# Performance work log

Hardware: AMD Instinct MI355X
Metric: run time of the kernel (lower is better)

The kernel has to match this reference:

```python
import jax, jax.numpy as jnp
import numpy as np

B, S, E = 8, 4096, 512
QKV, H = 512, 8
D = QKV // H  # head_dim = 64
EPS = 1e-6


def setup_inputs() -> dict:
    key = jax.random.key(0)
    ks = jax.random.split(key, 9)
    sc_in = 1.0 / np.sqrt(E)
    sc_qkv = 1.0 / np.sqrt(QKV)
    # Linear weights stored as [in, out] so y = x @ W + b (equivalent to torch x @ W_t.T + b)
    return {
        "x": jax.random.normal(ks[0], (B, S, E), dtype=jnp.float32),
        "Wq": jax.random.uniform(ks[1], (E, QKV), jnp.float32, -sc_in, sc_in),
        "bq": jax.random.uniform(ks[2], (QKV,), jnp.float32, -sc_in, sc_in),
        "Wk": jax.random.uniform(ks[3], (E, QKV), jnp.float32, -sc_in, sc_in),
        "bk": jax.random.uniform(ks[4], (QKV,), jnp.float32, -sc_in, sc_in),
        "Wv": jax.random.uniform(ks[5], (E, QKV), jnp.float32, -sc_in, sc_in),
        "bv": jax.random.uniform(ks[6], (QKV,), jnp.float32, -sc_in, sc_in),
        "Wo": jax.random.uniform(ks[7], (QKV, E), jnp.float32, -sc_qkv, sc_qkv),
        "bo": jax.random.uniform(ks[8], (E,), jnp.float32, -sc_qkv, sc_qkv),
    }


def feature_map(t):
    # elu(x) + 1 (always positive features)
    return jax.nn.elu(t) + 1.0


def reference(x, Wq, bq, Wk, bk, Wv, bv, Wo, bo):
    bs, seqlen, _ = x.shape
    q = (x @ Wq + bq).reshape(bs, seqlen, H, D)
    k = (x @ Wk + bk).reshape(bs, seqlen, H, D)
    v = (x @ Wv + bv).reshape(bs, seqlen, H, D)
    q = feature_map(q)
    k = feature_map(k)
    # kv: [n, h, m, d] -- per-head outer-product accumulation over sequence
    kv = jnp.einsum('nshd,nshm->nhmd', k, v)
    # normalizer z: [n, l, h]
    z = 1.0 / (jnp.einsum('nlhd,nhd->nlh', q, k.sum(axis=1)) + EPS)
    out = jnp.einsum('nlhd,nhmd,nlh->nlhm', q, kv, z)
    out = out.reshape(bs, seqlen, QKV)
    return out @ Wo + bo
```

## Files before the change

### kernel.cpp

```cpp
#include <hip/hip_runtime.h>
#include <hip/hip_bf16.h>


typedef __bf16 bf16x8 __attribute__((ext_vector_type(8)));
typedef float  f32x4  __attribute__((ext_vector_type(4)));

__device__ __forceinline__ float b2f(unsigned short u) {
    unsigned int x = ((unsigned int)u) << 16;
    return __builtin_bit_cast(float, x);
}
__device__ __forceinline__ unsigned short f2b(float f) {
    unsigned int u = __builtin_bit_cast(unsigned int, f);
    unsigned int r = (u + 0x7FFFu + ((u >> 16) & 1u)) >> 16;
    return (unsigned short)r;
}
__device__ __forceinline__ void load_lds16(const unsigned short* g, unsigned short* l) {
    __builtin_amdgcn_global_load_lds(
        (const __attribute__((address_space(1))) void*)g,
        (__attribute__((address_space(3))) void*)l, 16, 0, 0);
}

__global__ void prep_kernel(const float* __restrict__ x,
                            const float* __restrict__ w0, const float* __restrict__ w1,
                            const float* __restrict__ w2, const float* __restrict__ w3,
                            unsigned short* __restrict__ xb, unsigned short* __restrict__ wt) {
    __shared__ float tile[64][65];
    int t = threadIdx.x;
    if (blockIdx.x >= 256) {
        int i = (blockIdx.x - 256) * 256 + t;
        float4 v = ((const float4*)x)[i];
        ushort4 o;
        o.x = f2b(v.x); o.y = f2b(v.y); o.z = f2b(v.z); o.w = f2b(v.w);
        ((ushort4*)xb)[i] = o;
        return;
    }
    int idx = blockIdx.x;
    int bz = idx >> 6, by = (idx >> 3) & 7, bx = idx & 7;
    const float* src = (bz == 0) ? w0 : (bz == 1) ? w1 : (bz == 2) ? w2 : w3;
    unsigned short* dst = wt + (size_t)bz * 512 * 512;
    int rb = by * 64, cb = bx * 64;
    #pragma unroll
    for (int i = 0; i < 16; i++) {
        int c = t + i * 256; int r = c >> 6, cc = c & 63;
        tile[r][cc] = src[(rb + r) * 512 + cb + cc];
    }
    __syncthreads();
    #pragma unroll
    for (int i = 0; i < 16; i++) {
        int c = t + i * 256; int r = c >> 6, cc = c & 63;
        dst[(cb + r) * 512 + rb + cc] = f2b(tile[cc][r]);
    }
}

__device__ __forceinline__ void gemm128(const unsigned short* __restrict__ A,
                                        const unsigned short* __restrict__ Bt,
                                        const float* __restrict__ bias,
                                        unsigned short* __restrict__ Cout,
                                        int mtile, int ntile, bool act) {
    __shared__ __align__(16) unsigned short sA[128 * 64];
    __shared__ __align__(16) unsigned short sB[128 * 64];
    const int tid  = threadIdx.x;
    const int wave = tid >> 6, lane = tid & 63;
    const int wm = wave >> 1, wn = wave & 1;
    const int quad = lane >> 4, l16 = lane & 15;
    const int mbase = mtile * 128, nbase = ntile * 128;
    const int rsub = lane >> 3;
    const int coff = (((lane & 7) ^ rsub) << 3);

    f32x4 acc[4][4];
    #pragma unroll
    for (int i = 0; i < 4; i++)
        #pragma unroll
        for (int j = 0; j < 4; j++) acc[i][j] = (f32x4){0.f, 0.f, 0.f, 0.f};

    for (int kb = 0; kb < 512; kb += 64) {
        #pragma unroll
        for (int t = 0; t < 4; t++) {
            int r0 = t * 32 + wave * 8;
            load_lds16(&A[(size_t)(mbase + r0 + rsub) * 512 + kb + coff], &sA[r0 * 64]);
            load_lds16(&Bt[(size_t)(nbase + r0 + rsub) * 512 + kb + coff], &sB[r0 * 64]);
        }
        __syncthreads();
        #pragma unroll
        for (int ko = 0; ko < 64; ko += 32) {
            bf16x8 af[4], bfr[4];
            int pg = ((quad + (ko >> 3)) ^ (l16 & 7)) << 3;
            #pragma unroll
            for (int f = 0; f < 4; f++)
                af[f] = *(const bf16x8*)&sA[(wm * 64 + f * 16 + l16) * 64 + pg];
            #pragma unroll
            for (int f = 0; f < 4; f++)
                bfr[f] = *(const bf16x8*)&sB[(wn * 64 + f * 16 + l16) * 64 + pg];
            #pragma unroll
            for (int i = 0; i < 4; i++)
                #pragma unroll
                for (int j = 0; j < 4; j++)
                    acc[i][j] = __builtin_amdgcn_mfma_f32_16x16x32_bf16(af[i], bfr[j], acc[i][j], 0, 0, 0);
        }
        __syncthreads();
    }
    #pragma unroll
    for (int i = 0; i < 4; i++) {
        #pragma unroll
        for (int j = 0; j < 4; j++) {
            int gcol = nbase + wn * 64 + j * 16 + l16;
            float bv = bias[gcol];
            #pragma unroll
            for (int r = 0; r < 4; r++) {
                int grow = mbase + wm * 64 + i * 16 + quad * 4 + r;
                float v = acc[i][j][r] + bv;
                if (act) v = v > 0.f ? v + 1.f : __expf(v);
                Cout[(size_t)grow * 512 + gcol] = f2b(v);
            }
        }
    }
}

__global__ __launch_bounds__(256, 4) void gemm_qkv_kernel(
        const unsigned short* __restrict__ xb, const unsigned short* __restrict__ wt,
        const float* __restrict__ bq, const float* __restrict__ bk, const float* __restrict__ bv,
        unsigned short* __restrict__ qb, unsigned short* __restrict__ kb,
        unsigned short* __restrict__ vb) {
    int tensor = blockIdx.x >> 2, ntile = blockIdx.x & 3;
    const unsigned short* Bt = wt + (size_t)tensor * 512 * 512;
    const float* bias = tensor == 0 ? bq : tensor == 1 ? bk : bv;
    unsigned short* out = tensor == 0 ? qb : tensor == 1 ? kb : vb;
    gemm128(xb, Bt, bias, out, blockIdx.y, ntile, tensor < 2);
}

__global__ __launch_bounds__(256) void kv_kernel(
        const unsigned short* __restrict__ kb, const unsigned short* __restrict__ vb,
        float* __restrict__ kvp, float* __restrict__ ksp) {
    int bh = blockIdx.x, sc = blockIdx.y;
    int b = bh >> 3, h = bh & 7;
    const int tid = threadIdx.x;
    int wave = tid >> 6;
    int cell = tid & 63;
    int m0 = (cell >> 3) * 8, d0 = (cell & 7) * 8;
    __shared__ __align__(16) unsigned short sK[32 * 64];
    __shared__ __align__(16) unsigned short sV[32 * 64];
    __shared__ float sAcc[4096];
    __shared__ float sKs[64];
    float acc[8][8];
    #pragma unroll
    for (int i = 0; i < 8; i++)
        #pragma unroll
        for (int j = 0; j < 8; j++) acc[i][j] = 0.f;
    float ks = 0.f;
    size_t gbase = ((size_t)(b * 4096 + sc * 256)) * 512 + h * 64;

    for (int tile = 0; tile < 8; tile++) {
        {
            int r = tid >> 3, cc = (tid & 7) * 8;
            size_t g = gbase + (size_t)(tile * 32 + r) * 512 + cc;
            *(uint4*)&sK[r * 64 + cc] = *(const uint4*)&kb[g];
            *(uint4*)&sV[r * 64 + cc] = *(const uint4*)&vb[g];
        }
        __syncthreads();
        #pragma unroll
        for (int ss = 0; ss < 8; ss++) {
            int s = wave * 8 + ss;
            uint4 kr = *(const uint4*)&sK[s * 64 + d0];
            uint4 vr = *(const uint4*)&sV[s * 64 + m0];
            float kvals[8], vvals[8];
            const unsigned int* kp = (const unsigned int*)&kr;
            const unsigned int* vp = (const unsigned int*)&vr;
            #pragma unroll
            for (int i = 0; i < 4; i++) {
                kvals[2*i]   = __builtin_bit_cast(float, kp[i] << 16);
                kvals[2*i+1] = __builtin_bit_cast(float, kp[i] & 0xFFFF0000u);
                vvals[2*i]   = __builtin_bit_cast(float, vp[i] << 16);
                vvals[2*i+1] = __builtin_bit_cast(float, vp[i] & 0xFFFF0000u);
            }
            #pragma unroll
            for (int i = 0; i < 8; i++)
                #pragma unroll
                for (int j = 0; j < 8; j++)
                    acc[i][j] += vvals[i] * kvals[j];
            ks += b2f(sK[s * 64 + cell]);
        }
        __syncthreads();
    }
    for (int w = 0; w < 4; w++) {
        if (wave == w) {
            #pragma unroll
            for (int i = 0; i < 8; i++)
                #pragma unroll
                for (int j = 0; j < 8; j++) {
                    int idx = (m0 + i) * 64 + d0 + j;
                    if (w == 0) sAcc[idx] = acc[i][j];
                    else        sAcc[idx] += acc[i][j];
                }
            if (w == 0) sKs[cell] = ks;
            else        sKs[cell] += ks;
        }
        __syncthreads();
    }
    float* kvout = kvp + ((size_t)sc * 64 + bh) * 4096;
    #pragma unroll
    for (int i = 0; i < 16; i++) {
        int idx = tid + i * 256;
        kvout[idx] = sAcc[idx];
    }
    if (tid < 64) ksp[((size_t)sc * 64 + bh) * 64 + tid] = sKs[tid];
}

__global__ __launch_bounds__(256) void mid_kernel(
        const float* __restrict__ kvp, const float* __restrict__ ksp,
        const unsigned short* __restrict__ qb,
        unsigned short* __restrict__ kvb, float* __restrict__ zb) {
    int bh = blockIdx.x >> 3, chunk = blockIdx.x & 7;
    int b = bh >> 3, h = bh & 7;
    int tid = threadIdx.x;
    __shared__ float sKsum[64];
    if (tid < 64) {
        float s = 0.f;
        #pragma unroll
        for (int sc = 0; sc < 16; sc++) s += ksp[((size_t)sc * 64 + bh) * 64 + tid];
        sKsum[tid] = s;
    }
    __syncthreads();
    int seg = tid & 7, rsub = tid >> 3;
    float ks8[8];
    #pragma unroll
    for (int j = 0; j < 8; j++) ks8[j] = sKsum[seg * 8 + j];
    #pragma unroll
    for (int p = 0; p < 16; p++) {
        int row = chunk * 512 + p * 32 + rsub;
        uint4 w = *(const uint4*)&qb[((size_t)(b * 4096 + row)) * 512 + h * 64 + seg * 8];
        const unsigned int* qp = (const unsigned int*)&w;
        float d = 0.f;
        #pragma unroll
        for (int i = 0; i < 4; i++) {
            d += __builtin_bit_cast(float, qp[i] << 16)        * ks8[2*i];
            d += __builtin_bit_cast(float, qp[i] & 0xFFFF0000u) * ks8[2*i+1];
        }
        d += __shfl_xor(d, 1, 64);
        d += __shfl_xor(d, 2, 64);
        d += __shfl_xor(d, 4, 64);
        if (seg == 0) zb[h * 32768 + b * 4096 + row] = 1.f / (d + 1e-6f);
    }
    if (chunk == 0) {
        #pragma unroll
        for (int i = 0; i < 4; i++) {
            int idx = (tid + i * 256) * 4;
            float s0 = 0.f, s1 = 0.f, s2 = 0.f, s3 = 0.f;
            #pragma unroll
            for (int sc = 0; sc < 16; sc++) {
                float4 v = *(const float4*)&kvp[((size_t)sc * 64 + bh) * 4096 + idx];
                s0 += v.x; s1 += v.y; s2 += v.z; s3 += v.w;
            }
            ushort4 o; o.x = f2b(s0); o.y = f2b(s1); o.z = f2b(s2); o.w = f2b(s3);
            *(ushort4*)&kvb[(size_t)bh * 4096 + idx] = o;
        }
    }
}

__global__ __launch_bounds__(256, 2) void fused_out_kernel(
        const unsigned short* __restrict__ qb,
        const unsigned short* __restrict__ kvb, const float* __restrict__ zb,
        const unsigned short* __restrict__ wto, const float* __restrict__ bo,
        float* __restrict__ out) {
    __shared__ __align__(16) unsigned short sQ[128 * 64];
    __shared__ __align__(16) unsigned short sWo[128 * 64];
    __shared__ __align__(16) unsigned short sKV[64 * 64];
    __shared__ __align__(16) unsigned short sO1[128 * 64];
    __shared__ float sZ[128];
    const int tid  = threadIdx.x;
    const int wave = tid >> 6, lane = tid & 63;
    const int wm = wave >> 1, wn = wave & 1;
    const int quad = lane >> 4, l16 = lane & 15;
    const int mbase = blockIdx.y * 128, nbase = blockIdx.x * 128;
    const int b = blockIdx.y >> 5;
    const int rsub = lane >> 3;
    const int coff = (((lane & 7) ^ rsub) << 3);

    f32x4 accm[4][4];
    #pragma unroll
    for (int i = 0; i < 4; i++)
        #pragma unroll
        for (int j = 0; j < 4; j++) accm[i][j] = (f32x4){0.f, 0.f, 0.f, 0.f};

    for (int h = 0; h < 8; h++) {
        #pragma unroll
        for (int t = 0; t < 4; t++) {
            int r0 = t * 32 + wave * 8;
            load_lds16(&qb[(size_t)(mbase + r0 + rsub) * 512 + h * 64 + coff], &sQ[r0 * 64]);
            load_lds16(&wto[(size_t)(nbase + r0 + rsub) * 512 + h * 64 + coff], &sWo[r0 * 64]);
        }
        #pragma unroll
        for (int t = 0; t < 2; t++) {
            int r0 = t * 32 + wave * 8;
            load_lds16(&kvb[(size_t)(b * 8 + h) * 4096 + (r0 + rsub) * 64 + coff], &sKV[r0 * 64]);
        }
        if (tid < 128) sZ[tid] = zb[h * 32768 + mbase + tid];
        __syncthreads();
        f32x4 acco[4][2];
        #pragma unroll
        for (int f = 0; f < 4; f++)
            #pragma unroll
            for (int j = 0; j < 2; j++) acco[f][j] = (f32x4){0.f, 0.f, 0.f, 0.f};
        #pragma unroll
        for (int ko = 0; ko < 64; ko += 32) {
            bf16x8 af[4], bfr[2];
            int pg = ((quad + (ko >> 3)) ^ (l16 & 7)) << 3;
            #pragma unroll
            for (int f = 0; f < 4; f++)
                af[f] = *(const bf16x8*)&sQ[(wm * 64 + f * 16 + l16) * 64 + pg];
            #pragma unroll
            for (int j = 0; j < 2; j++)
                bfr[j] = *(const bf16x8*)&sKV[(wn * 32 + j * 16 + l16) * 64 + pg];
            #pragma unroll
            for (int f = 0; f < 4; f++)
                #pragma unroll
                for (int j = 0; j < 2; j++)
                    acco[f][j] = __builtin_amdgcn_mfma_f32_16x16x32_bf16(af[f], bfr[j], acco[f][j], 0, 0, 0);
        }
        #pragma unroll
        for (int f = 0; f < 4; f++)
            #pragma unroll
            for (int j = 0; j < 2; j++)
                #pragma unroll
                for (int r = 0; r < 4; r++) {
                    int row = wm * 64 + f * 16 + quad * 4 + r;
                    int col = wn * 32 + j * 16 + l16;
                    float v = acco[f][j][r] * sZ[row];
                    int g = col >> 3;
                    sO1[row * 64 + ((g ^ (row & 7)) << 3) + (col & 7)] = f2b(v);
                }
        __syncthreads();
        #pragma unroll
        for (int ko = 0; ko < 64; ko += 32) {
            bf16x8 af[4], bfr[4];
            int pg = ((quad + (ko >> 3)) ^ (l16 & 7)) << 3;
            #pragma unroll
            for (int f = 0; f < 4; f++)
                af[f] = *(const bf16x8*)&sO1[(wm * 64 + f * 16 + l16) * 64 + pg];
            #pragma unroll
            for (int f = 0; f < 4; f++)
                bfr[f] = *(const bf16x8*)&sWo[(wn * 64 + f * 16 + l16) * 64 + pg];
            #pragma unroll
            for (int i = 0; i < 4; i++)
                #pragma unroll
                for (int j = 0; j < 4; j++)
                    accm[i][j] = __builtin_amdgcn_mfma_f32_16x16x32_bf16(af[i], bfr[j], accm[i][j], 0, 0, 0);
        }
        __syncthreads();
    }
    #pragma unroll
    for (int i = 0; i < 4; i++)
        #pragma unroll
        for (int j = 0; j < 4; j++) {
            int gcol = nbase + wn * 64 + j * 16 + l16;
            float bv = bo[gcol];
            #pragma unroll
            for (int r = 0; r < 4; r++) {
                int grow = mbase + wm * 64 + i * 16 + quad * 4 + r;
                out[(size_t)grow * 512 + gcol] = accm[i][j][r] + bv;
            }
        }
}

extern "C" void kernel_launch(void* const* d_in, const int* in_sizes, int n_in,
                              void* d_out, int out_size, void* d_ws, size_t ws_size,
                              hipStream_t stream) {
    const float* x  = (const float*)d_in[0];
    const float* Wq = (const float*)d_in[1];
    const float* bq = (const float*)d_in[2];
    const float* Wk = (const float*)d_in[3];
    const float* bk = (const float*)d_in[4];
    const float* Wv = (const float*)d_in[5];
    const float* bv = (const float*)d_in[6];
    const float* Wo = (const float*)d_in[7];
    const float* bo = (const float*)d_in[8];
    float* out = (float*)d_out;

    char* wsb = (char*)d_ws;
    char* ob  = (char*)d_out;
    unsigned short* vb  = (unsigned short*)ob;
    unsigned short* xb  = (unsigned short*)(ob + 33554432ull);
    float*          kvp = (float*)(ob + 33554432ull);
    unsigned short* qb  = (unsigned short*)wsb;
    unsigned short* kb  = (unsigned short*)(wsb + 33554432ull);
    unsigned short* wt  = (unsigned short*)(wsb + 67108864ull);
    float*          ksp = (float*)(wsb + 69206016ull);
    unsigned short* kvb = (unsigned short*)(wsb + 69468160ull);
    float*          zb  = (float*)(wsb + 69992448ull);

    prep_kernel<<<16640, 256, 0, stream>>>(x, Wq, Wk, Wv, Wo, xb, wt);
    gemm_qkv_kernel<<<dim3(12, 256), 256, 0, stream>>>(xb, wt, bq, bk, bv, qb, kb, vb);
    kv_kernel<<<dim3(64, 16), 256, 0, stream>>>(kb, vb, kvp, ksp);
    mid_kernel<<<512, 256, 0, stream>>>(kvp, ksp, qb, kvb, zb);
    fused_out_kernel<<<dim3(4, 256), 256, 0, stream>>>(qb, kvb, zb,
            wt + 3ull * 512 * 512, bo, out);
}
```

Baseline: 288.1 us.

## Store K/V transposed, compute KV outer products with MFMA, remap blocks per XCD

```diff
diff --git a/kernel.cpp b/kernel.cpp
--- a/kernel.cpp
+++ b/kernel.cpp
@@ -52,11 +52,20 @@
     }
 }
 
-__device__ __forceinline__ void gemm128(const unsigned short* __restrict__ A,
-                                        const unsigned short* __restrict__ Bt,
-                                        const float* __restrict__ bias,
-                                        unsigned short* __restrict__ Cout,
-                                        int mtile, int ntile, bool act) {
+__global__ __launch_bounds__(256, 4) void gemm_qkv_kernel(
+        const unsigned short* __restrict__ xb, const unsigned short* __restrict__ wt,
+        const float* __restrict__ bq, const float* __restrict__ bk, const float* __restrict__ bv,
+        unsigned short* __restrict__ qb, unsigned short* __restrict__ kT,
+        unsigned short* __restrict__ vT) {
+    int g = blockIdx.x;
+    int xcd = g & 7, slot = g >> 3;
+    int mtile = xcd * 32 + slot / 12;
+    int tn = slot % 12;
+    int tensor = tn >> 2, ntile = tn & 3;
+    const unsigned short* Bt = wt + (size_t)tensor * 512 * 512;
+    const float* bias = tensor == 0 ? bq : tensor == 1 ? bk : bv;
+    bool act = tensor < 2;
+
     __shared__ __align__(16) unsigned short sA[128 * 64];
     __shared__ __align__(16) unsigned short sB[128 * 64];
     const int tid  = threadIdx.x;
@@ -77,7 +86,7 @@
         #pragma unroll
         for (int t = 0; t < 4; t++) {
             int r0 = t * 32 + wave * 8;
-            load_lds16(&A[(size_t)(mbase + r0 + rsub) * 512 + kb + coff], &sA[r0 * 64]);
+            load_lds16(&xb[(size_t)(mbase + r0 + rsub) * 512 + kb + coff], &sA[r0 * 64]);
             load_lds16(&Bt[(size_t)(nbase + r0 + rsub) * 512 + kb + coff], &sB[r0 * 64]);
         }
         __syncthreads();
@@ -99,110 +108,122 @@
         }
         __syncthreads();
     }
-    #pragma unroll
-    for (int i = 0; i < 4; i++) {
-        #pragma unroll
-        for (int j = 0; j < 4; j++) {
-            int gcol = nbase + wn * 64 + j * 16 + l16;
-            float bv = bias[gcol];
+    if (tensor == 0) {
+        #pragma unroll
+        for (int i = 0; i < 4; i++)
+            #pragma unroll
+            for (int j = 0; j < 4; j++) {
+                int gcol = nbase + wn * 64 + j * 16 + l16;
+                float bv = bias[gcol];
+                #pragma unroll
+                for (int r = 0; r < 4; r++) {
+                    int grow = mbase + wm * 64 + i * 16 + quad * 4 + r;
+                    float v = acc[i][j][r] + bv;
+                    v = v > 0.f ? v + 1.f : __expf(v);
+                    qb[(size_t)grow * 512 + gcol] = f2b(v);
+                }
+            }
+    } else {
+        unsigned short* T = (tensor == 1) ? kT : vT;
+        #pragma unroll
+        for (int i = 0; i < 4; i++)
+            #pragma unroll
+            for (int j = 0; j < 4; j++) {
+                int gcol = nbase + wn * 64 + j * 16 + l16;
+                int h = gcol >> 6, d = gcol & 63;
+                float bv = bias[gcol];
+                int grow0 = mbase + wm * 64 + i * 16 + quad * 4;
+                int b = grow0 >> 12, s0 = grow0 & 4095;
+                ushort4 o;
+                #pragma unroll
+                for (int r = 0; r < 4; r++) {
+                    float v = acc[i][j][r] + bv;
+                    if (act) v = v > 0.f ? v + 1.f : __expf(v);
+                    ((unsigned short*)&o)[r] = f2b(v);
+                }
+                *(ushort4*)&T[(((size_t)b * 8 + h) * 64 + d) * 4096 + s0] = o;
+            }
+    }
+}
+
+__global__ __launch_bounds__(256, 4) void kv_kernel(
+        const unsigned short* __restrict__ kT, const unsigned short* __restrict__ vT,
+        float* __restrict__ kvp, float* __restrict__ ksp) {
+    int bh = blockIdx.x >> 4, sc = blockIdx.x & 15;
+    const int tid = threadIdx.x;
+    const int wave = tid >> 6, lane = tid & 63;
+    const int wm = wave >> 1, wn = wave & 1;
+    const int quad = lane >> 4, l16 = lane & 15;
+    const int rsub = lane >> 3;
+    const int coff = (((lane & 7) ^ rsub) << 3);
+    __shared__ __align__(16) unsigned short sV[64 * 64];
+    __shared__ __align__(16) unsigned short sK[64 * 64];
+    __shared__ float sKs[256];
+
+    f32x4 acc[2][2];
+    #pragma unroll
+    for (int i = 0; i < 2; i++)
+        #pragma unroll
+        for (int j = 0; j < 2; j++) acc[i][j] = (f32x4){0.f, 0.f, 0.f, 0.f};
+    float ks = 0.f;
+    const int dks = tid >> 2, sgks = tid & 3;
+    size_t base = (size_t)bh * 64 * 4096 + sc * 256;
+
+    for (int kb = 0; kb < 4; kb++) {
+        int s0 = kb * 64;
+        #pragma unroll
+        for (int t = 0; t < 2; t++) {
+            int r0 = t * 32 + wave * 8;
+            load_lds16(&vT[base + (size_t)(r0 + rsub) * 4096 + s0 + coff], &sV[r0 * 64]);
+            load_lds16(&kT[base + (size_t)(r0 + rsub) * 4096 + s0 + coff], &sK[r0 * 64]);
+        }
+        __syncthreads();
+        #pragma unroll
+        for (int gi = 0; gi < 2; gi++) {
+            int gg = sgks * 2 + gi;
+            int pg = ((gg ^ (dks & 7)) << 3);
+            uint4 w = *(const uint4*)&sK[dks * 64 + pg];
+            const unsigned int* wp = (const unsigned int*)&w;
+            #pragma unroll
+            for (int i2 = 0; i2 < 4; i2++) {
+                ks += __builtin_bit_cast(float, wp[i2] << 16);
+                ks += __builtin_bit_cast(float, wp[i2] & 0xFFFF0000u);
+            }
+        }
+        #pragma unroll
+        for (int ko = 0; ko < 64; ko += 32) {
+            bf16x8 af[2], bfr[2];
+            int pg = ((quad + (ko >> 3)) ^ (l16 & 7)) << 3;
+            #pragma unroll
+            for (int f = 0; f < 2; f++)
+                af[f] = *(const bf16x8*)&sV[(wm * 32 + f * 16 + l16) * 64 + pg];
+            #pragma unroll
+            for (int f = 0; f < 2; f++)
+                bfr[f] = *(const bf16x8*)&sK[(wn * 32 + f * 16 + l16) * 64 + pg];
+            #pragma unroll
+            for (int i = 0; i < 2; i++)
+                #pragma unroll
+                for (int j = 0; j < 2; j++)
+                    acc[i][j] = __builtin_amdgcn_mfma_f32_16x16x32_bf16(af[i], bfr[j], acc[i][j], 0, 0, 0);
+        }
+        __syncthreads();
+    }
+    float* kvout = kvp + ((size_t)sc * 64 + bh) * 4096;
+    #pragma unroll
+    for (int i = 0; i < 2; i++)
+        #pragma unroll
+        for (int j = 0; j < 2; j++)
             #pragma unroll
             for (int r = 0; r < 4; r++) {
-                int grow = mbase + wm * 64 + i * 16 + quad * 4 + r;
-                float v = acc[i][j][r] + bv;
-                if (act) v = v > 0.f ? v + 1.f : __expf(v);
-                Cout[(size_t)grow * 512 + gcol] = f2b(v);
-            }
-        }
-    }
-}
-
-__global__ __launch_bounds__(256, 4) void gemm_qkv_kernel(
-        const unsigned short* __restrict__ xb, const unsigned short* __restrict__ wt,
-        const float* __restrict__ bq, const float* __restrict__ bk, const float* __restrict__ bv,
-        unsigned short* __restrict__ qb, unsigned short* __restrict__ kb,
-        unsigned short* __restrict__ vb) {
-    int tensor = blockIdx.x >> 2, ntile = blockIdx.x & 3;
-    const unsigned short* Bt = wt + (size_t)tensor * 512 * 512;
-    const float* bias = tensor == 0 ? bq : tensor == 1 ? bk : bv;
-    unsigned short* out = tensor == 0 ? qb : tensor == 1 ? kb : vb;
-    gemm128(xb, Bt, bias, out, blockIdx.y, ntile, tensor < 2);
-}
-
-__global__ __launch_bounds__(256) void kv_kernel(
-        const unsigned short* __restrict__ kb, const unsigned short* __restrict__ vb,
-        float* __restrict__ kvp, float* __restrict__ ksp) {
-    int bh = blockIdx.x, sc = blockIdx.y;
-    int b = bh >> 3, h = bh & 7;
-    const int tid = threadIdx.x;
-    int wave = tid >> 6;
-    int cell = tid & 63;
-    int m0 = (cell >> 3) * 8, d0 = (cell & 7) * 8;
-    __shared__ __align__(16) unsigned short sK[32 * 64];
-    __shared__ __align__(16) unsigned short sV[32 * 64];
-    __shared__ float sAcc[4096];
-    __shared__ float sKs[64];
-    float acc[8][8];
-    #pragma unroll
-    for (int i = 0; i < 8; i++)
-        #pragma unroll
-        for (int j = 0; j < 8; j++) acc[i][j] = 0.f;
-    float ks = 0.f;
-    size_t gbase = ((size_t)(b * 4096 + sc * 256)) * 512 + h * 64;
-
-    for (int tile = 0; tile < 8; tile++) {
-        {
-            int r = tid >> 3, cc = (tid & 7) * 8;
-            size_t g = gbase + (size_t)(tile * 32 + r) * 512 + cc;
-            *(uint4*)&sK[r * 64 + cc] = *(const uint4*)&kb[g];
-            *(uint4*)&sV[r * 64 + cc] = *(const uint4*)&vb[g];
-        }
-        __syncthreads();
-        #pragma unroll
-        for (int ss = 0; ss < 8; ss++) {
-            int s = wave * 8 + ss;
-            uint4 kr = *(const uint4*)&sK[s * 64 + d0];
-            uint4 vr = *(const uint4*)&sV[s * 64 + m0];
-            float kvals[8], vvals[8];
-            const unsigned int* kp = (const unsigned int*)&kr;
-            const unsigned int* vp = (const unsigned int*)&vr;
-            #pragma unroll
-            for (int i = 0; i < 4; i++) {
-                kvals[2*i]   = __builtin_bit_cast(float, kp[i] << 16);
-                kvals[2*i+1] = __builtin_bit_cast(float, kp[i] & 0xFFFF0000u);
-                vvals[2*i]   = __builtin_bit_cast(float, vp[i] << 16);
-                vvals[2*i+1] = __builtin_bit_cast(float, vp[i] & 0xFFFF0000u);
-            }
-            #pragma unroll
-            for (int i = 0; i < 8; i++)
-                #pragma unroll
-                for (int j = 0; j < 8; j++)
-                    acc[i][j] += vvals[i] * kvals[j];
-            ks += b2f(sK[s * 64 + cell]);
-        }
-        __syncthreads();
-    }
-    for (int w = 0; w < 4; w++) {
-        if (wave == w) {
-            #pragma unroll
-            for (int i = 0; i < 8; i++)
-                #pragma unroll
-                for (int j = 0; j < 8; j++) {
-                    int idx = (m0 + i) * 64 + d0 + j;
-                    if (w == 0) sAcc[idx] = acc[i][j];
-                    else        sAcc[idx] += acc[i][j];
-                }
-            if (w == 0) sKs[cell] = ks;
-            else        sKs[cell] += ks;
-        }
-        __syncthreads();
-    }
-    float* kvout = kvp + ((size_t)sc * 64 + bh) * 4096;
-    #pragma unroll
-    for (int i = 0; i < 16; i++) {
-        int idx = tid + i * 256;
-        kvout[idx] = sAcc[idx];
-    }
-    if (tid < 64) ksp[((size_t)sc * 64 + bh) * 64 + tid] = sKs[tid];
+                int m = wm * 32 + i * 16 + quad * 4 + r;
+                int d = wn * 32 + j * 16 + l16;
+                kvout[m * 64 + d] = acc[i][j][r];
+            }
+    sKs[tid] = ks;
+    __syncthreads();
+    if (tid < 64)
+        ksp[((size_t)sc * 64 + bh) * 64 + tid] =
+            sKs[tid * 4] + sKs[tid * 4 + 1] + sKs[tid * 4 + 2] + sKs[tid * 4 + 3];
 }
 
 __global__ __launch_bounds__(256) void mid_kernel(
@@ -261,6 +282,11 @@
         const unsigned short* __restrict__ kvb, const float* __restrict__ zb,
         const unsigned short* __restrict__ wto, const float* __restrict__ bo,
         float* __restrict__ out) {
+    int g = blockIdx.x;
+    int xcd = g & 7, slot = g >> 3;
+    int mtile = xcd * 32 + (slot >> 2);
+    int ntile = slot & 3;
+
     __shared__ __align__(16) unsigned short sQ[128 * 64];
     __shared__ __align__(16) unsigned short sWo[128 * 64];
     __shared__ __align__(16) unsigned short sKV[64 * 64];
@@ -270,8 +296,8 @@
     const int wave = tid >> 6, lane = tid & 63;
     const int wm = wave >> 1, wn = wave & 1;
     const int quad = lane >> 4, l16 = lane & 15;
-    const int mbase = blockIdx.y * 128, nbase = blockIdx.x * 128;
-    const int b = blockIdx.y >> 5;
+    const int mbase = mtile * 128, nbase = ntile * 128;
+    const int b = mtile >> 5;
     const int rsub = lane >> 3;
     const int coff = (((lane & 7) ^ rsub) << 3);
 
@@ -325,8 +351,8 @@
                     int row = wm * 64 + f * 16 + quad * 4 + r;
                     int col = wn * 32 + j * 16 + l16;
                     float v = acco[f][j][r] * sZ[row];
-                    int g = col >> 3;
-                    sO1[row * 64 + ((g ^ (row & 7)) << 3) + (col & 7)] = f2b(v);
+                    int grp = col >> 3;
+                    sO1[row * 64 + ((grp ^ (row & 7)) << 3) + (col & 7)] = f2b(v);
                 }
         __syncthreads();
         #pragma unroll
@@ -377,20 +403,20 @@
 
     char* wsb = (char*)d_ws;
     char* ob  = (char*)d_out;
-    unsigned short* vb  = (unsigned short*)ob;
+    unsigned short* vT  = (unsigned short*)ob;
     unsigned short* xb  = (unsigned short*)(ob + 33554432ull);
     float*          kvp = (float*)(ob + 33554432ull);
     unsigned short* qb  = (unsigned short*)wsb;
-    unsigned short* kb  = (unsigned short*)(wsb + 33554432ull);
+    unsigned short* kT  = (unsigned short*)(wsb + 33554432ull);
     unsigned short* wt  = (unsigned short*)(wsb + 67108864ull);
     float*          ksp = (float*)(wsb + 69206016ull);
     unsigned short* kvb = (unsigned short*)(wsb + 69468160ull);
     float*          zb  = (float*)(wsb + 69992448ull);
 
     prep_kernel<<<16640, 256, 0, stream>>>(x, Wq, Wk, Wv, Wo, xb, wt);
-    gemm_qkv_kernel<<<dim3(12, 256), 256, 0, stream>>>(xb, wt, bq, bk, bv, qb, kb, vb);
-    kv_kernel<<<dim3(64, 16), 256, 0, stream>>>(kb, vb, kvp, ksp);
+    gemm_qkv_kernel<<<3072, 256, 0, stream>>>(xb, wt, bq, bk, bv, qb, kT, vT);
+    kv_kernel<<<1024, 256, 0, stream>>>(kT, vT, kvp, ksp);
     mid_kernel<<<512, 256, 0, stream>>>(kvp, ksp, qb, kvb, zb);
-    fused_out_kernel<<<dim3(4, 256), 256, 0, stream>>>(qb, kvb, zb,
+    fused_out_kernel<<<1024, 256, 0, stream>>>(qb, kvb, zb,
             wt + 3ull * 512 * 512, bo, out);
 }
```

Measured after the change: 263.7 us. -8.5%, faster.
